# Kernel optimization log

Measured on AMD Instinct MI355X. Metric: run time of the kernel, lower is better.

## Reference

```python
import jax, jax.numpy as jnp
import numpy as np

SEQ = 2048
DIM = 2048
GROUPS = 8
GROUP_SIZE = 4
DQK = DIM // (GROUPS * GROUP_SIZE)  # 64 (also dim_v)


def _glorot(key, shape):
    # Faithful to source: dim_in = prod(shape[-1]) == shape[-1], so sigma = 1/sqrt(shape[-1])
    sigma = np.sqrt(2.0 / (shape[-1] + shape[-1])).astype(np.float32)
    return jax.random.normal(key, shape, dtype=jnp.float32) * sigma


def rope(x):
    """RoPE on last axis; x: [..., seq, dim]. Closed-form per-pair rotation."""
    seq, dim = x.shape[-2], x.shape[-1]
    half = dim // 2
    # angle[s, j] = s * 10000^(-2j/dim)
    inv_freq = 10000.0 ** (-2.0 * jnp.arange(half, dtype=jnp.float32) / dim)
    ang = jnp.arange(seq, dtype=jnp.float32)[:, None] * inv_freq[None, :]  # [seq, half]
    c, s = jnp.cos(ang), jnp.sin(ang)
    xp = x.reshape(*x.shape[:-1], half, 2)
    x1, x2 = xp[..., 0], xp[..., 1]
    out = jnp.stack([c * x1 - s * x2, s * x1 + c * x2], axis=-1)
    return out.reshape(x.shape)


def setup_inputs() -> dict:
    key = jax.random.key(0)
    kx, kq, kk, kv, ko = jax.random.split(key, 5)
    return {
        "x": jax.random.normal(kx, (SEQ, DIM), dtype=jnp.float32),
        "w_query": _glorot(kq, (GROUPS, GROUP_SIZE, DIM, DQK)),
        "w_key": _glorot(kk, (GROUPS, DIM, DQK)),
        "w_value": _glorot(kv, (GROUPS, DIM, DQK)),
        "w_out": _glorot(ko, (GROUPS, GROUP_SIZE, DQK, DIM)),
    }


def reference(x, w_query, w_key, w_value, w_out):
    seq = x.shape[0]
    dqk = w_query.shape[-1]
    # projections: g=groups, h=group_size (query heads per group)
    q = rope(jnp.einsum('sd,ghdk->ghsk', x, w_query))  # [g,h,seq,dqk]
    k = rope(jnp.einsum('sd,gdk->gsk', x, w_key))      # [g,seq,dqk]
    v = jnp.einsum('sd,gdv->gsv', x, w_value)          # [g,seq,dv]
    scores = jnp.einsum('ghsk,gtk->ghst', q, k) / jnp.sqrt(jnp.float32(dqk))
    causal = jnp.tril(jnp.ones((seq, seq), dtype=bool))  # log(tril(ones)) == 0 / -inf
    scores = jnp.where(causal, scores, -jnp.inf)
    probs = jax.nn.softmax(scores, axis=-1)
    o = jnp.einsum('ghst,gtv->ghsv', probs, v)
    # per-head out-proj then sum over (g, h)
    return jnp.einsum('ghsv,ghvd->sd', o, w_out)
```

## Files before the change

kernel.cpp:

```cpp
#include <hip/hip_runtime.h>
#include <hip/hip_bf16.h>

#define SEQ 2048
#define DIMM 2048
#define NQH 32
#define NKVH 8
#define HD 64

typedef _Float16 half8 __attribute__((ext_vector_type(8)));
typedef float f32x4 __attribute__((ext_vector_type(4)));
using fp16 = _Float16;

typedef __attribute__((address_space(1))) unsigned int ga_u32;
typedef __attribute__((address_space(3))) unsigned int ls_u32;

__device__ __forceinline__ void gll16(const void* g, void* l) {
    __builtin_amdgcn_global_load_lds((const ga_u32*)g, (ls_u32*)l, 16, 0, 0);
}

__global__ void cast_f32_f16(const float* __restrict__ in, fp16* __restrict__ out, int n) {
    int i = (blockIdx.x * 256 + threadIdx.x) * 4;
    if (i < n) {
        float4 v = *reinterpret_cast<const float4*>(in + i);
#pragma unroll
        for (int j = 0; j < 4; j++) out[i + j] = (fp16)(&v.x)[j];
    }
}

__global__ void transpose_qkvw(const float* __restrict__ wq, const float* __restrict__ wk,
                               const float* __restrict__ wv, fp16* __restrict__ out) {
    __shared__ float tile[64][65];
    const int z = blockIdx.z;
    const float* inh = (z < 32) ? wq + (size_t)z * SEQ * HD
                                : (z < 40) ? wk + (size_t)(z - 32) * SEQ * HD
                                           : wv + (size_t)(z - 40) * SEQ * HD;
    fp16* outh = out + (size_t)z * HD * SEQ;
    int r0 = blockIdx.x * 64;
    int t = threadIdx.x;
#pragma unroll
    for (int i = 0; i < 16; i++) {
        int idx = i * 256 + t;
        int r = idx >> 6, c = idx & 63;
        tile[r][c] = inh[(size_t)(r0 + r) * HD + c];
    }
    __syncthreads();
#pragma unroll
    for (int i = 0; i < 16; i++) {
        int idx = i * 256 + t;
        int cc = idx >> 6, rr = idx & 63;
        outh[(size_t)cc * SEQ + r0 + rr] = (fp16)tile[rr][cc];
    }
}

__global__ void transpose_cast(const float* __restrict__ in, fp16* __restrict__ out, int R, int C) {
    __shared__ float tile[64][65];
    int r0 = blockIdx.x * 64, c0 = blockIdx.y * 64;
    int t = threadIdx.x;
#pragma unroll
    for (int i = 0; i < 16; i++) {
        int idx = i * 256 + t;
        int r = idx >> 6, c = idx & 63;
        tile[r][c] = in[(size_t)(r0 + r) * C + c0 + c];
    }
    __syncthreads();
#pragma unroll
    for (int i = 0; i < 16; i++) {
        int idx = i * 256 + t;
        int cc = idx >> 6, rr = idx & 63;
        out[(size_t)(c0 + cc) * R + r0 + rr] = (fp16)tile[rr][cc];
    }
}

__global__ void rope_vt_kernel(const fp16* __restrict__ proj, fp16* __restrict__ qb,
                               fp16* __restrict__ kb, fp16* __restrict__ vtb) {
    __shared__ fp16 tile[64][72];
    const int bx = blockIdx.x;
    if (bx < 10240) {
        int tid = bx * 256 + threadIdx.x;
        int pair = tid & 31;
        int s = (tid >> 5) & 2047;
        int head = tid >> 16;
        const fp16* src = proj + (size_t)s * 3072 + head * HD + 2 * pair;
        float x1 = (float)src[0];
        float x2 = (float)src[1];
        float invf = expf(-((float)pair / 32.0f) * 9.210340371976184f);
        float ang = (float)s * invf;
        float sn, cs;
        sincosf(ang, &sn, &cs);
        float o1 = cs * x1 - sn * x2;
        float o2 = sn * x1 + cs * x2;
        fp16* dst = (head < NQH) ? (qb + ((size_t)head * SEQ + s) * HD + 2 * pair)
                                 : (kb + ((size_t)(head - NQH) * SEQ + s) * HD + 2 * pair);
        dst[0] = (fp16)o1;
        dst[1] = (fp16)o2;
    } else {
        const int idx = bx - 10240;
        const int g = idx >> 5;
        const int s0 = (idx & 31) * 64;
        const int t = threadIdx.x;
#pragma unroll
        for (int i = 0; i < 16; i++) {
            int id2 = i * 256 + t;
            int r = id2 >> 6, c = id2 & 63;
            tile[r][c] = proj[(size_t)(s0 + r) * 3072 + 2560 + g * HD + c];
        }
        __syncthreads();
#pragma unroll
        for (int i = 0; i < 16; i++) {
            int id2 = i * 256 + t;
            int cc = id2 >> 6, rr = id2 & 63;
            vtb[((size_t)g * HD + cc) * SEQ + s0 + rr] = tile[rr][cc];
        }
    }
}

template <int BM, int BN, int WF32>
__global__ __launch_bounds__(256) void gemm_tpl(
    const fp16* __restrict__ A, const fp16* __restrict__ Bt, void* __restrict__ Cout, int Nout) {
    __shared__ fp16 As[2][BM][64];
    __shared__ fp16 Bs[2][BN][64];
    const int t = threadIdx.x;
    const int m0 = blockIdx.x * BM, n0 = blockIdx.y * BN;
    const int wid = t >> 6, lane = t & 63;
    const int wm = (wid >> 1) * (BM / 2), wn = (wid & 1) * (BN / 2);
    const int lr = lane & 15, lg = lane >> 4;
    constexpr int MR = BM / 32, NR = BN / 32;
    f32x4 acc[MR][NR] = {};
    auto stage_ = [&](int kt, int b) {
#pragma unroll
        for (int s = t; s < BM * 8; s += 256) {
            int row = s >> 3, ch = s & 7;
            int lch = ch ^ (row & 7);
            gll16(A + (size_t)(m0 + row) * 2048 + (kt << 6) + lch * 8,
                  (char*)&As[b][0][0] + s * 16);
        }
#pragma unroll
        for (int s = t; s < BN * 8; s += 256) {
            int row = s >> 3, ch = s & 7;
            int lch = ch ^ (row & 7);
            gll16(Bt + (size_t)(n0 + row) * 2048 + (kt << 6) + lch * 8,
                  (char*)&Bs[b][0][0] + s * 16);
        }
    };
    stage_(0, 0);
    __syncthreads();
    for (int kt = 0; kt < 32; ++kt) {
        const int cur = kt & 1;
        if (kt + 1 < 32) stage_(kt + 1, cur ^ 1);
#pragma unroll
        for (int kk = 0; kk < 2; kk++) {
            half8 af[MR], bfv[NR];
#pragma unroll
            for (int m = 0; m < MR; m++) {
                int row = wm + m * 16 + lr;
                af[m] = *(const half8*)((const char*)&As[cur][row][0] +
                                        (((kk * 4 + lg) ^ (row & 7)) * 16));
            }
#pragma unroll
            for (int n = 0; n < NR; n++) {
                int row = wn + n * 16 + lr;
                bfv[n] = *(const half8*)((const char*)&Bs[cur][row][0] +
                                         (((kk * 4 + lg) ^ (row & 7)) * 16));
            }
            __builtin_amdgcn_s_setprio(1);
#pragma unroll
            for (int m = 0; m < MR; m++)
#pragma unroll
                for (int n = 0; n < NR; n++)
                    acc[m][n] = __builtin_amdgcn_mfma_f32_16x16x32_f16(af[m], bfv[n], acc[m][n], 0, 0, 0);
            __builtin_amdgcn_s_setprio(0);
        }
        __syncthreads();
    }
#pragma unroll
    for (int m = 0; m < MR; m++)
#pragma unroll
        for (int n = 0; n < NR; n++)
#pragma unroll
            for (int r = 0; r < 4; r++) {
                int row = m0 + wm + m * 16 + lg * 4 + r;
                int col = n0 + wn + n * 16 + lr;
                if (WF32)
                    ((float*)Cout)[(size_t)row * Nout + col] = acc[m][n][r];
                else
                    ((fp16*)Cout)[(size_t)row * Nout + col] = (fp16)acc[m][n][r];
            }
}

__global__ __launch_bounds__(256) void attn_kernel(
    const fp16* __restrict__ qb, const fp16* __restrict__ kb,
    const fp16* __restrict__ vt, fp16* __restrict__ o_all) {
    __shared__ fp16 Kb[2][64][64];
    __shared__ fp16 Vb[2][64][64];
    __shared__ fp16 P[4][16][64];
    const int t = threadIdx.x, wid = t >> 6, lane = t & 63;
    const int bx = blockIdx.x;
    const int grp = bx >> 5;
    const int a = grp & 7;
    const int sel = grp >> 3;
    const int qt = (sel == 0) ? (31 - a) : (sel == 1) ? (8 + a) : (sel == 2) ? (23 - a) : a;
    const int head = bx & 31;
    const int g = head >> 2;
    const int lr = lane & 15, lg = lane >> 4;
    const fp16* qh = qb + (size_t)head * SEQ * HD;
    const fp16* kh = kb + (size_t)g * SEQ * HD;
    const fp16* vh = vt + (size_t)g * HD * SEQ;
    const int srow = lane >> 3, schunk = lane & 7;
    const int qr0 = qt * 64 + wid * 16;

    half8 aq0 = *reinterpret_cast<const half8*>(qh + (size_t)(qr0 + lr) * HD + lg * 8);
    half8 aq1 = *reinterpret_cast<const half8*>(qh + (size_t)(qr0 + lr) * HD + 32 + lg * 8);
#pragma unroll
    for (int e = 0; e < 8; e++) {
        aq0[e] *= (fp16)0.125f;
        aq1[e] *= (fp16)0.125f;
    }
    f32x4 o[4] = {};
    float m[4], lsum[4];
#pragma unroll
    for (int r = 0; r < 4; r++) { m[r] = -1e30f; lsum[r] = 0.0f; }
    const int nt = qt + 1;

    auto stage = [&](int kt, int b) {
        const int kv0 = kt << 6;
#pragma unroll
        for (int i = 0; i < 2; ++i) {
            int row = wid * 16 + i * 8 + srow;
            int sw = (schunk ^ srow) * 8;
            gll16(kh + (size_t)(kv0 + row) * HD + sw, &Kb[b][wid * 16 + i * 8][0]);
            gll16(vh + (size_t)row * SEQ + kv0 + sw, &Vb[b][wid * 16 + i * 8][0]);
        }
    };

    stage(0, 0);
    __syncthreads();
    for (int tt = 0; tt < nt; ++tt) {
        const int cur = tt & 1;
        if (tt + 1 < nt) stage(tt + 1, cur ^ 1);
        const int kv0 = tt << 6;
        f32x4 sc[4];
        __builtin_amdgcn_s_setprio(1);
#pragma unroll
        for (int f = 0; f < 4; ++f) {
            int row = f * 16 + lr;
            const char* kbp = (const char*)&Kb[cur][row][0];
            half8 b0 = *(const half8*)(kbp + (((lg) ^ (row & 7)) * 16));
            half8 b1 = *(const half8*)(kbp + (((4 + lg) ^ (row & 7)) * 16));
            f32x4 s = {};
            s = __builtin_amdgcn_mfma_f32_16x16x32_f16(aq0, b0, s, 0, 0, 0);
            s = __builtin_amdgcn_mfma_f32_16x16x32_f16(aq1, b1, s, 0, 0, 0);
            sc[f] = s;
        }
        __builtin_amdgcn_s_setprio(0);
        if (tt == qt) {
#pragma unroll
            for (int f = 0; f < 4; f++)
#pragma unroll
                for (int r = 0; r < 4; r++) {
                    int q = qr0 + lg * 4 + r, kv = kv0 + f * 16 + lr;
                    if (kv > q) sc[f][r] = -1e30f;
                }
        }
        float lmax[4];
        bool ok = true;
#pragma unroll
        for (int r = 0; r < 4; r++) {
            lmax[r] = fmaxf(fmaxf(sc[0][r], sc[1][r]), fmaxf(sc[2][r], sc[3][r]));
            ok = ok && (lmax[r] <= m[r] + 8.0f);
        }
        if (!__all(ok)) {
#pragma unroll
            for (int r = 0; r < 4; r++) {
                float v = lmax[r];
                v = fmaxf(v, __shfl_xor(v, 1));
                v = fmaxf(v, __shfl_xor(v, 2));
                v = fmaxf(v, __shfl_xor(v, 4));
                v = fmaxf(v, __shfl_xor(v, 8));
                float mn = fmaxf(m[r], v);
                float alpha = __expf(m[r] - mn);
                m[r] = mn;
                lsum[r] *= alpha;
#pragma unroll
                for (int vf = 0; vf < 4; vf++) o[vf][r] *= alpha;
            }
        }
#pragma unroll
        for (int f = 0; f < 4; f++)
#pragma unroll
            for (int r = 0; r < 4; r++) {
                float p = __expf(sc[f][r] - m[r]);
                sc[f][r] = p;
                lsum[r] += p;
            }
        {
            char* pb = (char*)&P[wid][0][0];
#pragma unroll
            for (int f = 0; f < 4; f++)
#pragma unroll
                for (int r = 0; r < 4; r++) {
                    int row = lg * 4 + r, col = f * 16 + lr;
                    *(fp16*)(pb + row * 128 + (((col >> 3) ^ (row & 7)) * 16) + (col & 7) * 2) =
                        (fp16)sc[f][r];
                }
        }
        __builtin_amdgcn_s_setprio(1);
#pragma unroll
        for (int half = 0; half < 2; half++) {
            const char* pb = (const char*)&P[wid][0][0];
            half8 pa = *(const half8*)(pb + lr * 128 + (((half * 4 + lg) ^ (lr & 7)) * 16));
#pragma unroll
            for (int vf = 0; vf < 4; vf++) {
                int d = vf * 16 + lr;
                int xo = ((half * 4 + lg) ^ (d & 7)) * 16;
                half8 bv = *(const half8*)((const char*)&Vb[cur][d][0] + xo);
                o[vf] = __builtin_amdgcn_mfma_f32_16x16x32_f16(pa, bv, o[vf], 0, 0, 0);
            }
        }
        __builtin_amdgcn_s_setprio(0);
        __syncthreads();
    }
#pragma unroll
    for (int r = 0; r < 4; r++) {
        float v = lsum[r];
        v += __shfl_xor(v, 1);
        v += __shfl_xor(v, 2);
        v += __shfl_xor(v, 4);
        v += __shfl_xor(v, 8);
        lsum[r] = v;
    }
#pragma unroll
    for (int vf = 0; vf < 4; vf++)
#pragma unroll
        for (int r = 0; r < 4; r++) {
            float v = o[vf][r] / lsum[r];
            o_all[(size_t)(qr0 + lg * 4 + r) * 2048 + head * 64 + vf * 16 + lr] = (fp16)v;
        }
}

extern "C" void kernel_launch(void* const* d_in, const int* in_sizes, int n_in,
                              void* d_out, int out_size, void* d_ws, size_t ws_size,
                              hipStream_t stream) {
    const float* x  = (const float*)d_in[0];
    const float* wq = (const float*)d_in[1];
    const float* wk = (const float*)d_in[2];
    const float* wv = (const float*)d_in[3];
    const float* wo = (const float*)d_in[4];
    float* out = (float*)d_out;
    char* ws = (char*)d_ws;

    fp16* xh    = (fp16*)(ws);
    fp16* w2t   = xh;
    fp16* wqkvt = (fp16*)(ws + ((size_t)8 << 20));
    fp16* proj  = (fp16*)(ws + ((size_t)20 << 20));
    fp16* o_all = proj;
    fp16* qbuf  = (fp16*)(ws + ((size_t)32 << 20));
    fp16* kbuf  = (fp16*)(ws + ((size_t)40 << 20));
    fp16* vtb   = (fp16*)(ws + ((size_t)42 << 20));

    cast_f32_f16<<<dim3(4096), 256, 0, stream>>>(x, xh, SEQ * DIMM);
    transpose_qkvw<<<dim3(32, 1, 48), 256, 0, stream>>>(wq, wk, wv, wqkvt);
    gemm_tpl<64, 128, 0><<<dim3(32, 24), 256, 0, stream>>>(xh, wqkvt, proj, 3072);
    rope_vt_kernel<<<dim3(10496), 256, 0, stream>>>(proj, qbuf, kbuf, vtb);
    transpose_cast<<<dim3(32, 32), 256, 0, stream>>>(wo, w2t, 2048, 2048);
    attn_kernel<<<dim3(1024), 256, 0, stream>>>(qbuf, kbuf, vtb, o_all);
    gemm_tpl<64, 128, 1><<<dim3(32, 16), 256, 0, stream>>>(o_all, w2t, out, 2048);
}
```

Baseline: 144.0 us.

## Fuse weight prep kernels and restructure attention softmax with transposed scores and exp2

The x cast, QKV weight transpose and output weight transpose are merged into one prep kernel, which removes two launches and lets the output-weight transpose run before the QKV GEMM using its own buffer. The softmax scale and log2(e) factor are folded into Q during the RoPE pass, so attention uses exp2f and no longer rescales Q in fp16. The QK^T MFMA operands are swapped so each lane holds one query row. That makes the row max a two-step shuffle, shrinks the running max and sum to scalars, and lets P be written to LDS as packed stores. Risks include fp16 rounding with the larger Q scale and extra shuffles to broadcast alpha and 1/l.

```diff
diff --git a/kernel.cpp b/kernel.cpp
--- a/kernel.cpp
+++ b/kernel.cpp
@@ -9,6 +9,7 @@
 
 typedef _Float16 half8 __attribute__((ext_vector_type(8)));
 typedef float f32x4 __attribute__((ext_vector_type(4)));
+typedef __fp16 fp16raw2 __attribute__((ext_vector_type(2)));
 using fp16 = _Float16;
 
 typedef __attribute__((address_space(1))) unsigned int ga_u32;
@@ -18,56 +19,59 @@
     __builtin_amdgcn_global_load_lds((const ga_u32*)g, (ls_u32*)l, 16, 0, 0);
 }
 
-__global__ void cast_f32_f16(const float* __restrict__ in, fp16* __restrict__ out, int n) {
-    int i = (blockIdx.x * 256 + threadIdx.x) * 4;
-    if (i < n) {
-        float4 v = *reinterpret_cast<const float4*>(in + i);
-#pragma unroll
-        for (int j = 0; j < 4; j++) out[i + j] = (fp16)(&v.x)[j];
-    }
-}
-
-__global__ void transpose_qkvw(const float* __restrict__ wq, const float* __restrict__ wk,
-                               const float* __restrict__ wv, fp16* __restrict__ out) {
+__global__ void prep_kernel(const float* __restrict__ x,
+                            const float* __restrict__ wq, const float* __restrict__ wk,
+                            const float* __restrict__ wv, const float* __restrict__ wo,
+                            fp16* __restrict__ xh, fp16* __restrict__ wqkvt,
+                            fp16* __restrict__ w2t) {
     __shared__ float tile[64][65];
-    const int z = blockIdx.z;
-    const float* inh = (z < 32) ? wq + (size_t)z * SEQ * HD
-                                : (z < 40) ? wk + (size_t)(z - 32) * SEQ * HD
-                                           : wv + (size_t)(z - 40) * SEQ * HD;
-    fp16* outh = out + (size_t)z * HD * SEQ;
-    int r0 = blockIdx.x * 64;
-    int t = threadIdx.x;
-#pragma unroll
-    for (int i = 0; i < 16; i++) {
-        int idx = i * 256 + t;
-        int r = idx >> 6, c = idx & 63;
-        tile[r][c] = inh[(size_t)(r0 + r) * HD + c];
-    }
-    __syncthreads();
-#pragma unroll
-    for (int i = 0; i < 16; i++) {
-        int idx = i * 256 + t;
-        int cc = idx >> 6, rr = idx & 63;
-        outh[(size_t)cc * SEQ + r0 + rr] = (fp16)tile[rr][cc];
-    }
-}
-
-__global__ void transpose_cast(const float* __restrict__ in, fp16* __restrict__ out, int R, int C) {
-    __shared__ float tile[64][65];
-    int r0 = blockIdx.x * 64, c0 = blockIdx.y * 64;
-    int t = threadIdx.x;
-#pragma unroll
-    for (int i = 0; i < 16; i++) {
-        int idx = i * 256 + t;
-        int r = idx >> 6, c = idx & 63;
-        tile[r][c] = in[(size_t)(r0 + r) * C + c0 + c];
-    }
-    __syncthreads();
-#pragma unroll
-    for (int i = 0; i < 16; i++) {
-        int idx = i * 256 + t;
-        int cc = idx >> 6, rr = idx & 63;
-        out[(size_t)(c0 + cc) * R + r0 + rr] = (fp16)tile[rr][cc];
+    const int bx = blockIdx.x;
+    const int t = threadIdx.x;
+    if (bx < 1024) {
+#pragma unroll
+        for (int it = 0; it < 4; it++) {
+            int i = bx * 4096 + it * 1024 + t * 4;
+            float4 v = *reinterpret_cast<const float4*>(x + i);
+            fp16* o = xh + i;
+            o[0] = (fp16)v.x; o[1] = (fp16)v.y; o[2] = (fp16)v.z; o[3] = (fp16)v.w;
+        }
+    } else if (bx < 2560) {
+        const int zi = bx - 1024;
+        const int z = zi >> 5;
+        const int r0 = (zi & 31) * 64;
+        const float* inh = (z < 32) ? wq + (size_t)z * SEQ * HD
+                                    : (z < 40) ? wk + (size_t)(z - 32) * SEQ * HD
+                                               : wv + (size_t)(z - 40) * SEQ * HD;
+        fp16* outh = wqkvt + (size_t)z * HD * SEQ;
+#pragma unroll
+        for (int i = 0; i < 16; i++) {
+            int idx = i * 256 + t;
+            int r = idx >> 6, c = idx & 63;
+            tile[r][c] = inh[(size_t)(r0 + r) * HD + c];
+        }
+        __syncthreads();
+#pragma unroll
+        for (int i = 0; i < 16; i++) {
+            int idx = i * 256 + t;
+            int cc = idx >> 6, rr = idx & 63;
+            outh[(size_t)cc * SEQ + r0 + rr] = (fp16)tile[rr][cc];
+        }
+    } else {
+        const int zi = bx - 2560;
+        const int r0 = (zi >> 5) * 64, c0 = (zi & 31) * 64;
+#pragma unroll
+        for (int i = 0; i < 16; i++) {
+            int idx = i * 256 + t;
+            int r = idx >> 6, c = idx & 63;
+            tile[r][c] = wo[(size_t)(r0 + r) * 2048 + c0 + c];
+        }
+        __syncthreads();
+#pragma unroll
+        for (int i = 0; i < 16; i++) {
+            int idx = i * 256 + t;
+            int cc = idx >> 6, rr = idx & 63;
+            w2t[(size_t)(c0 + cc) * 2048 + r0 + rr] = (fp16)tile[rr][cc];
+        }
     }
 }
 
@@ -89,8 +93,14 @@
         sincosf(ang, &sn, &cs);
         float o1 = cs * x1 - sn * x2;
         float o2 = sn * x1 + cs * x2;
-        fp16* dst = (head < NQH) ? (qb + ((size_t)head * SEQ + s) * HD + 2 * pair)
-                                 : (kb + ((size_t)(head - NQH) * SEQ + s) * HD + 2 * pair);
+        fp16* dst;
+        if (head < NQH) {
+            o1 *= 0.18033688011112042f;
+            o2 *= 0.18033688011112042f;
+            dst = qb + ((size_t)head * SEQ + s) * HD + 2 * pair;
+        } else {
+            dst = kb + ((size_t)(head - NQH) * SEQ + s) * HD + 2 * pair;
+        }
         dst[0] = (fp16)o1;
         dst[1] = (fp16)o2;
     } else {
@@ -207,18 +217,12 @@
     const fp16* vh = vt + (size_t)g * HD * SEQ;
     const int srow = lane >> 3, schunk = lane & 7;
     const int qr0 = qt * 64 + wid * 16;
+    char* pb = (char*)&P[wid][0][0];
 
     half8 aq0 = *reinterpret_cast<const half8*>(qh + (size_t)(qr0 + lr) * HD + lg * 8);
     half8 aq1 = *reinterpret_cast<const half8*>(qh + (size_t)(qr0 + lr) * HD + 32 + lg * 8);
-#pragma unroll
-    for (int e = 0; e < 8; e++) {
-        aq0[e] *= (fp16)0.125f;
-        aq1[e] *= (fp16)0.125f;
-    }
     f32x4 o[4] = {};
-    float m[4], lsum[4];
-#pragma unroll
-    for (int r = 0; r < 4; r++) { m[r] = -1e30f; lsum[r] = 0.0f; }
+    float m_ = -1e30f, lsum_ = 0.0f;
     const int nt = qt + 1;
 
     auto stage = [&](int kt, int b) {
@@ -247,71 +251,64 @@
             half8 b0 = *(const half8*)(kbp + (((lg) ^ (row & 7)) * 16));
             half8 b1 = *(const half8*)(kbp + (((4 + lg) ^ (row & 7)) * 16));
             f32x4 s = {};
-            s = __builtin_amdgcn_mfma_f32_16x16x32_f16(aq0, b0, s, 0, 0, 0);
-            s = __builtin_amdgcn_mfma_f32_16x16x32_f16(aq1, b1, s, 0, 0, 0);
+            s = __builtin_amdgcn_mfma_f32_16x16x32_f16(b0, aq0, s, 0, 0, 0);
+            s = __builtin_amdgcn_mfma_f32_16x16x32_f16(b1, aq1, s, 0, 0, 0);
             sc[f] = s;
         }
         __builtin_amdgcn_s_setprio(0);
         if (tt == qt) {
+            const int q = qr0 + lr;
 #pragma unroll
             for (int f = 0; f < 4; f++)
 #pragma unroll
                 for (int r = 0; r < 4; r++) {
-                    int q = qr0 + lg * 4 + r, kv = kv0 + f * 16 + lr;
+                    int kv = kv0 + f * 16 + lg * 4 + r;
                     if (kv > q) sc[f][r] = -1e30f;
                 }
         }
-        float lmax[4];
-        bool ok = true;
-#pragma unroll
-        for (int r = 0; r < 4; r++) {
-            lmax[r] = fmaxf(fmaxf(sc[0][r], sc[1][r]), fmaxf(sc[2][r], sc[3][r]));
-            ok = ok && (lmax[r] <= m[r] + 8.0f);
-        }
-        if (!__all(ok)) {
-#pragma unroll
-            for (int r = 0; r < 4; r++) {
-                float v = lmax[r];
-                v = fmaxf(v, __shfl_xor(v, 1));
-                v = fmaxf(v, __shfl_xor(v, 2));
-                v = fmaxf(v, __shfl_xor(v, 4));
-                v = fmaxf(v, __shfl_xor(v, 8));
-                float mn = fmaxf(m[r], v);
-                float alpha = __expf(m[r] - mn);
-                m[r] = mn;
-                lsum[r] *= alpha;
-#pragma unroll
-                for (int vf = 0; vf < 4; vf++) o[vf][r] *= alpha;
-            }
-        }
+        float lmax = sc[0][0];
 #pragma unroll
         for (int f = 0; f < 4; f++)
 #pragma unroll
-            for (int r = 0; r < 4; r++) {
-                float p = __expf(sc[f][r] - m[r]);
-                sc[f][r] = p;
-                lsum[r] += p;
-            }
-        {
-            char* pb = (char*)&P[wid][0][0];
-#pragma unroll
-            for (int f = 0; f < 4; f++)
-#pragma unroll
-                for (int r = 0; r < 4; r++) {
-                    int row = lg * 4 + r, col = f * 16 + lr;
-                    *(fp16*)(pb + row * 128 + (((col >> 3) ^ (row & 7)) * 16) + (col & 7) * 2) =
-                        (fp16)sc[f][r];
-                }
+            for (int r = 0; r < 4; r++) lmax = fmaxf(lmax, sc[f][r]);
+        if (!__all(lmax <= m_ + 11.0f)) {
+            float v = lmax;
+            v = fmaxf(v, __shfl_xor(v, 16));
+            v = fmaxf(v, __shfl_xor(v, 32));
+            float mn = fmaxf(m_, v);
+            float alpha = exp2f(m_ - mn);
+            m_ = mn;
+            lsum_ *= alpha;
+            float al[4];
+#pragma unroll
+            for (int r = 0; r < 4; r++) al[r] = __shfl(alpha, lg * 4 + r);
+#pragma unroll
+            for (int vf = 0; vf < 4; vf++)
+#pragma unroll
+                for (int r = 0; r < 4; r++) o[vf][r] *= al[r];
+        }
+#pragma unroll
+        for (int f = 0; f < 4; f++) {
+            float p0 = exp2f(sc[f][0] - m_);
+            float p1 = exp2f(sc[f][1] - m_);
+            float p2 = exp2f(sc[f][2] - m_);
+            float p3 = exp2f(sc[f][3] - m_);
+            lsum_ += (p0 + p1) + (p2 + p3);
+            fp16raw2 k0 = __builtin_amdgcn_cvt_pkrtz(p0, p1);
+            fp16raw2 k1 = __builtin_amdgcn_cvt_pkrtz(p2, p3);
+            uint2 w;
+            w.x = __builtin_bit_cast(unsigned int, k0);
+            w.y = __builtin_bit_cast(unsigned int, k1);
+            *(uint2*)(pb + lr * 128 + ((f * 32 + lg * 8) ^ ((lr & 7) << 4))) = w;
         }
         __builtin_amdgcn_s_setprio(1);
 #pragma unroll
-        for (int half = 0; half < 2; half++) {
-            const char* pb = (const char*)&P[wid][0][0];
-            half8 pa = *(const half8*)(pb + lr * 128 + (((half * 4 + lg) ^ (lr & 7)) * 16));
+        for (int h = 0; h < 2; h++) {
+            half8 pa = *(const half8*)(pb + lr * 128 + (((h * 4 + lg) ^ (lr & 7)) * 16));
 #pragma unroll
             for (int vf = 0; vf < 4; vf++) {
                 int d = vf * 16 + lr;
-                int xo = ((half * 4 + lg) ^ (d & 7)) * 16;
+                int xo = ((h * 4 + lg) ^ (d & 7)) * 16;
                 half8 bv = *(const half8*)((const char*)&Vb[cur][d][0] + xo);
                 o[vf] = __builtin_amdgcn_mfma_f32_16x16x32_f16(pa, bv, o[vf], 0, 0, 0);
             }
@@ -319,20 +316,16 @@
         __builtin_amdgcn_s_setprio(0);
         __syncthreads();
     }
-#pragma unroll
-    for (int r = 0; r < 4; r++) {
-        float v = lsum[r];
-        v += __shfl_xor(v, 1);
-        v += __shfl_xor(v, 2);
-        v += __shfl_xor(v, 4);
-        v += __shfl_xor(v, 8);
-        lsum[r] = v;
-    }
+    lsum_ += __shfl_xor(lsum_, 16);
+    lsum_ += __shfl_xor(lsum_, 32);
+    float li[4];
+#pragma unroll
+    for (int r = 0; r < 4; r++) li[r] = 1.0f / __shfl(lsum_, lg * 4 + r);
 #pragma unroll
     for (int vf = 0; vf < 4; vf++)
 #pragma unroll
         for (int r = 0; r < 4; r++) {
-            float v = o[vf][r] / lsum[r];
+            float v = o[vf][r] * li[r];
             o_all[(size_t)(qr0 + lg * 4 + r) * 2048 + head * 64 + vf * 16 + lr] = (fp16)v;
         }
 }
@@ -349,19 +342,17 @@
     char* ws = (char*)d_ws;
 
     fp16* xh    = (fp16*)(ws);
-    fp16* w2t   = xh;
     fp16* wqkvt = (fp16*)(ws + ((size_t)8 << 20));
     fp16* proj  = (fp16*)(ws + ((size_t)20 << 20));
     fp16* o_all = proj;
-    fp16* qbuf  = (fp16*)(ws + ((size_t)32 << 20));
-    fp16* kbuf  = (fp16*)(ws + ((size_t)40 << 20));
-    fp16* vtb   = (fp16*)(ws + ((size_t)42 << 20));
-
-    cast_f32_f16<<<dim3(4096), 256, 0, stream>>>(x, xh, SEQ * DIMM);
-    transpose_qkvw<<<dim3(32, 1, 48), 256, 0, stream>>>(wq, wk, wv, wqkvt);
+    fp16* w2t   = (fp16*)(ws + ((size_t)32 << 20));
+    fp16* qbuf  = (fp16*)(ws + ((size_t)40 << 20));
+    fp16* kbuf  = (fp16*)(ws + ((size_t)48 << 20));
+    fp16* vtb   = (fp16*)(ws + ((size_t)50 << 20));
+
+    prep_kernel<<<dim3(3584), 256, 0, stream>>>(x, wq, wk, wv, wo, xh, wqkvt, w2t);
     gemm_tpl<64, 128, 0><<<dim3(32, 24), 256, 0, stream>>>(xh, wqkvt, proj, 3072);
     rope_vt_kernel<<<dim3(10496), 256, 0, stream>>>(proj, qbuf, kbuf, vtb);
-    transpose_cast<<<dim3(32, 32), 256, 0, stream>>>(wo, w2t, 2048, 2048);
     attn_kernel<<<dim3(1024), 256, 0, stream>>>(qbuf, kbuf, vtb, o_all);
     gemm_tpl<64, 128, 1><<<dim3(32, 16), 256, 0, stream>>>(o_all, w2t, out, 2048);
 }
```

Measured after the change: 133.8 us. -7.1%, faster.
